# Optimization experiments

Hardware: AMD Instinct MI355X
Metric: run time of the kernel (lower is better)

## Reference

```python
import jax, jax.numpy as jnp
import numpy as np

TEMPERATURE = 100.0

def setup_inputs() -> dict:
    key = jax.random.key(0)
    n, d = 8192, 4096
    grad = jax.random.normal(key, (n, d), dtype=jnp.float32)
    return {"grad": grad}

def reference(grad) -> jnp.ndarray:
    # scores_i = sum_j (G @ G^T)_{ij} = G_i . (sum_j G_j)  -- avoids [n,n] gram
    colsum = jnp.sum(grad, axis=0)                 # [d]
    scores = grad @ colsum                         # [n]
    w = jax.nn.softmax(scores / TEMPERATURE, axis=0)  # softmax over rows (dim=0)
    # weighted row pooling: sum_i w_i * G_i -> [d]
    return w @ grad
```

## Files before the change

### kernel.cpp

```cpp
#include <hip/hip_runtime.h>
#include <math.h>

#define NROWS 8192
#define NCOLS 4096
#define TEMPERATURE 100.0f

#define ROW_CHUNKS 128
#define ROWS_PER_CHUNK (NROWS / ROW_CHUNKS)

__global__ __launch_bounds__(256)
void colsum_kernel(const float* __restrict__ g, float* __restrict__ colsum) {
    const int col  = (blockIdx.x * 256 + threadIdx.x) * 4;
    const int row0 = blockIdx.y * ROWS_PER_CHUNK;
    const float* p = g + (size_t)row0 * NCOLS + col;
    float4 acc = make_float4(0.f, 0.f, 0.f, 0.f);
    #pragma unroll 4
    for (int r = 0; r < ROWS_PER_CHUNK; ++r) {
        float4 v = *reinterpret_cast<const float4*>(p);
        acc.x += v.x; acc.y += v.y; acc.z += v.z; acc.w += v.w;
        p += NCOLS;
    }
    atomicAdd(&colsum[col + 0], acc.x);
    atomicAdd(&colsum[col + 1], acc.y);
    atomicAdd(&colsum[col + 2], acc.z);
    atomicAdd(&colsum[col + 3], acc.w);
}

__global__ __launch_bounds__(256)
void scores_kernel(const float* __restrict__ g, const float* __restrict__ colsum,
                   float* __restrict__ scores) {
    __shared__ float cs[NCOLS];
    for (int i = threadIdx.x; i < NCOLS / 4; i += 256) {
        reinterpret_cast<float4*>(cs)[i] =
            reinterpret_cast<const float4*>(colsum)[i];
    }
    __syncthreads();

    const int wave = threadIdx.x >> 6;
    const int lane = threadIdx.x & 63;
    const int row  = blockIdx.x * 4 + wave;
    const float* p = g + (size_t)row * NCOLS;

    float acc = 0.f;
    #pragma unroll
    for (int k = 0; k < NCOLS / 256; ++k) {
        const int c = k * 256 + lane * 4;
        float4 v = *reinterpret_cast<const float4*>(p + c);
        float4 w = *reinterpret_cast<const float4*>(cs + c);
        acc += v.x * w.x + v.y * w.y + v.z * w.z + v.w * w.w;
    }
    #pragma unroll
    for (int off = 32; off > 0; off >>= 1) acc += __shfl_xor(acc, off, 64);
    if (lane == 0) scores[row] = acc;
}

__global__ __launch_bounds__(1024)
void softmax_kernel(const float* __restrict__ scores, float* __restrict__ w) {
    __shared__ float red[16];
    const int tid = threadIdx.x;

    float local[8];
    float m = -INFINITY;
    #pragma unroll
    for (int k = 0; k < 8; ++k) {
        local[k] = scores[tid + k * 1024];
        m = fmaxf(m, local[k]);
    }
    #pragma unroll
    for (int off = 32; off > 0; off >>= 1) m = fmaxf(m, __shfl_xor(m, off, 64));
    if ((tid & 63) == 0) red[tid >> 6] = m;
    __syncthreads();
    float gm = red[0];
    #pragma unroll
    for (int i = 1; i < 16; ++i) gm = fmaxf(gm, red[i]);
    __syncthreads();

    float e[8];
    float s = 0.f;
    #pragma unroll
    for (int k = 0; k < 8; ++k) {
        e[k] = __expf((local[k] - gm) * (1.0f / TEMPERATURE));
        s += e[k];
    }
    #pragma unroll
    for (int off = 32; off > 0; off >>= 1) s += __shfl_xor(s, off, 64);
    if ((tid & 63) == 0) red[tid >> 6] = s;
    __syncthreads();
    float total = 0.f;
    #pragma unroll
    for (int i = 0; i < 16; ++i) total += red[i];

    const float inv = 1.0f / total;
    #pragma unroll
    for (int k = 0; k < 8; ++k) w[tid + k * 1024] = e[k] * inv;
}

__global__ __launch_bounds__(256)
void pool_kernel(const float* __restrict__ g, const float* __restrict__ w,
                 float* __restrict__ out) {
    const int col  = (blockIdx.x * 256 + threadIdx.x) * 4;
    const int row0 = blockIdx.y * ROWS_PER_CHUNK;
    const float* p = g + (size_t)row0 * NCOLS + col;
    float4 acc = make_float4(0.f, 0.f, 0.f, 0.f);
    #pragma unroll 4
    for (int r = 0; r < ROWS_PER_CHUNK; ++r) {
        const float wt = w[row0 + r];
        float4 v = *reinterpret_cast<const float4*>(p);
        acc.x += wt * v.x; acc.y += wt * v.y;
        acc.z += wt * v.z; acc.w += wt * v.w;
        p += NCOLS;
    }
    atomicAdd(&out[col + 0], acc.x);
    atomicAdd(&out[col + 1], acc.y);
    atomicAdd(&out[col + 2], acc.z);
    atomicAdd(&out[col + 3], acc.w);
}

extern "C" void kernel_launch(void* const* d_in, const int* in_sizes, int n_in,
                              void* d_out, int out_size, void* d_ws, size_t ws_size,
                              hipStream_t stream) {
    const float* grad = (const float*)d_in[0];
    float* out = (float*)d_out;

    float* colsum = (float*)d_ws;
    float* scores = colsum + NCOLS;
    float* wgt    = scores + NROWS;

    hipMemsetAsync(colsum, 0, NCOLS * sizeof(float), stream);
    hipMemsetAsync(out, 0, NCOLS * sizeof(float), stream);

    dim3 grid1(NCOLS / 1024, ROW_CHUNKS);
    colsum_kernel<<<grid1, 256, 0, stream>>>(grad, colsum);

    scores_kernel<<<NROWS / 4, 256, 0, stream>>>(grad, colsum, scores);

    softmax_kernel<<<1, 1024, 0, stream>>>(scores, wgt);

    pool_kernel<<<grid1, 256, 0, stream>>>(grad, wgt, out);
}
```

Measured before the change: 252.1 us.

## Replace atomic column reductions with partial-sum buffers plus separate reduce kernels

Column sums and the weighted pooling now use 2048 blocks of 16 rows each, and every block writes its own partial row into a workspace buffer. A dedicated reduce kernel then sums the 512 partials, which removes the float atomics and the two memsets. The scores kernel now processes two rows per wave, and the pool kernel stages its weights in shared memory. In exchange, each reduction adds an extra 8 MB partial-buffer write and read plus two more kernel launches.

Result: no change. 249.3 us (-1.1%).

```diff
diff --git a/kernel.cpp b/kernel.cpp
--- a/kernel.cpp
+++ b/kernel.cpp
@@ -3,55 +3,85 @@
 
 #define NROWS 8192
 #define NCOLS 4096
-#define TEMPERATURE 100.0f
+#define NCOLS4 (NCOLS / 4)
+#define TEMP_INV 0.01f
 
-#define ROW_CHUNKS 128
-#define ROWS_PER_CHUNK (NROWS / ROW_CHUNKS)
+#define STRIPS 4
+#define CHUNKS 512
+#define CHUNK_ROWS (NROWS / CHUNKS)
+#define STREAM_BLKS (STRIPS * CHUNKS)
 
 __global__ __launch_bounds__(256)
-void colsum_kernel(const float* __restrict__ g, float* __restrict__ colsum) {
-    const int col  = (blockIdx.x * 256 + threadIdx.x) * 4;
-    const int row0 = blockIdx.y * ROWS_PER_CHUNK;
-    const float* p = g + (size_t)row0 * NCOLS + col;
+void colsum_partial_kernel(const float* __restrict__ g,
+                           float* __restrict__ partial) {
+    const int strip = blockIdx.x & (STRIPS - 1);
+    const int chunk = blockIdx.x >> 2;
+    const int col   = strip * 1024 + threadIdx.x * 4;
+    const float* p  = g + (size_t)chunk * CHUNK_ROWS * NCOLS + col;
     float4 acc = make_float4(0.f, 0.f, 0.f, 0.f);
-    #pragma unroll 4
-    for (int r = 0; r < ROWS_PER_CHUNK; ++r) {
+    #pragma unroll
+    for (int r = 0; r < CHUNK_ROWS; ++r) {
         float4 v = *reinterpret_cast<const float4*>(p);
         acc.x += v.x; acc.y += v.y; acc.z += v.z; acc.w += v.w;
         p += NCOLS;
     }
-    atomicAdd(&colsum[col + 0], acc.x);
-    atomicAdd(&colsum[col + 1], acc.y);
-    atomicAdd(&colsum[col + 2], acc.z);
-    atomicAdd(&colsum[col + 3], acc.w);
+    *reinterpret_cast<float4*>(partial + (size_t)chunk * NCOLS + col) = acc;
+}
+
+__global__ __launch_bounds__(256)
+void reduce_kernel(const float* __restrict__ partial, float* __restrict__ dst) {
+    const int tid = threadIdx.x;
+    const int f4  = blockIdx.x * 16 + (tid & 15);
+    const int grp = tid >> 4;
+    const float4* p4 = reinterpret_cast<const float4*>(partial);
+    float4 acc = make_float4(0.f, 0.f, 0.f, 0.f);
+    for (int c = grp; c < CHUNKS; c += 16) {
+        float4 v = p4[(size_t)c * NCOLS4 + f4];
+        acc.x += v.x; acc.y += v.y; acc.z += v.z; acc.w += v.w;
+    }
+    __shared__ float4 red[256];
+    red[tid] = acc;
+    __syncthreads();
+    #pragma unroll
+    for (int s = 128; s >= 16; s >>= 1) {
+        if (tid < s) {
+            float4 o = red[tid + s];
+            red[tid].x += o.x; red[tid].y += o.y;
+            red[tid].z += o.z; red[tid].w += o.w;
+        }
+        __syncthreads();
+    }
+    if (tid < 16)
+        reinterpret_cast<float4*>(dst)[blockIdx.x * 16 + tid] = red[tid];
 }
 
 __global__ __launch_bounds__(256)
 void scores_kernel(const float* __restrict__ g, const float* __restrict__ colsum,
                    float* __restrict__ scores) {
-    __shared__ float cs[NCOLS];
-    for (int i = threadIdx.x; i < NCOLS / 4; i += 256) {
-        reinterpret_cast<float4*>(cs)[i] =
-            reinterpret_cast<const float4*>(colsum)[i];
-    }
+    __shared__ float4 cs4[NCOLS4];
+    for (int i = threadIdx.x; i < NCOLS4; i += 256)
+        cs4[i] = reinterpret_cast<const float4*>(colsum)[i];
     __syncthreads();
 
     const int wave = threadIdx.x >> 6;
     const int lane = threadIdx.x & 63;
-    const int row  = blockIdx.x * 4 + wave;
-    const float* p = g + (size_t)row * NCOLS;
-
-    float acc = 0.f;
     #pragma unroll
-    for (int k = 0; k < NCOLS / 256; ++k) {
-        const int c = k * 256 + lane * 4;
-        float4 v = *reinterpret_cast<const float4*>(p + c);
-        float4 w = *reinterpret_cast<const float4*>(cs + c);
-        acc += v.x * w.x + v.y * w.y + v.z * w.z + v.w * w.w;
+    for (int rr = 0; rr < 2; ++rr) {
+        const int row = blockIdx.x * 8 + wave * 2 + rr;
+        const float4* gp = reinterpret_cast<const float4*>(g)
+                         + (size_t)row * NCOLS4;
+        float acc = 0.f;
+        #pragma unroll
+        for (int k = 0; k < 16; ++k) {
+            const int idx = k * 64 + lane;
+            float4 v = gp[idx];
+            float4 c = cs4[idx];
+            acc += v.x * c.x + v.y * c.y + v.z * c.z + v.w * c.w;
+        }
+        #pragma unroll
+        for (int off = 32; off; off >>= 1) acc += __shfl_xor(acc, off, 64);
+        if (lane == 0) scores[row] = acc;
     }
-    #pragma unroll
-    for (int off = 32; off > 0; off >>= 1) acc += __shfl_xor(acc, off, 64);
-    if (lane == 0) scores[row] = acc;
 }
 
 __global__ __launch_bounds__(1024)
@@ -67,7 +97,7 @@
         m = fmaxf(m, local[k]);
     }
     #pragma unroll
-    for (int off = 32; off > 0; off >>= 1) m = fmaxf(m, __shfl_xor(m, off, 64));
+    for (int off = 32; off; off >>= 1) m = fmaxf(m, __shfl_xor(m, off, 64));
     if ((tid & 63) == 0) red[tid >> 6] = m;
     __syncthreads();
     float gm = red[0];
@@ -79,11 +109,11 @@
     float s = 0.f;
     #pragma unroll
     for (int k = 0; k < 8; ++k) {
-        e[k] = __expf((local[k] - gm) * (1.0f / TEMPERATURE));
+        e[k] = __expf((local[k] - gm) * TEMP_INV);
         s += e[k];
     }
     #pragma unroll
-    for (int off = 32; off > 0; off >>= 1) s += __shfl_xor(s, off, 64);
+    for (int off = 32; off; off >>= 1) s += __shfl_xor(s, off, 64);
     if ((tid & 63) == 0) red[tid >> 6] = s;
     __syncthreads();
     float total = 0.f;
@@ -96,24 +126,28 @@
 }
 
 __global__ __launch_bounds__(256)
-void pool_kernel(const float* __restrict__ g, const float* __restrict__ w,
-                 float* __restrict__ out) {
-    const int col  = (blockIdx.x * 256 + threadIdx.x) * 4;
-    const int row0 = blockIdx.y * ROWS_PER_CHUNK;
-    const float* p = g + (size_t)row0 * NCOLS + col;
+void pool_partial_kernel(const float* __restrict__ g, const float* __restrict__ w,
+                         float* __restrict__ partial) {
+    const int strip = blockIdx.x & (STRIPS - 1);
+    const int chunk = blockIdx.x >> 2;
+
+    __shared__ float wsm[CHUNK_ROWS];
+    if (threadIdx.x < CHUNK_ROWS)
+        wsm[threadIdx.x] = w[chunk * CHUNK_ROWS + threadIdx.x];
+    __syncthreads();
+
+    const int col  = strip * 1024 + threadIdx.x * 4;
+    const float* p = g + (size_t)chunk * CHUNK_ROWS * NCOLS + col;
     float4 acc = make_float4(0.f, 0.f, 0.f, 0.f);
-    #pragma unroll 4
-    for (int r = 0; r < ROWS_PER_CHUNK; ++r) {
-        const float wt = w[row0 + r];
+    #pragma unroll
+    for (int r = 0; r < CHUNK_ROWS; ++r) {
+        const float wt = wsm[r];
         float4 v = *reinterpret_cast<const float4*>(p);
         acc.x += wt * v.x; acc.y += wt * v.y;
         acc.z += wt * v.z; acc.w += wt * v.w;
         p += NCOLS;
     }
-    atomicAdd(&out[col + 0], acc.x);
-    atomicAdd(&out[col + 1], acc.y);
-    atomicAdd(&out[col + 2], acc.z);
-    atomicAdd(&out[col + 3], acc.w);
+    *reinterpret_cast<float4*>(partial + (size_t)chunk * NCOLS + col) = acc;
 }
 
 extern "C" void kernel_launch(void* const* d_in, const int* in_sizes, int n_in,
@@ -122,19 +156,15 @@
     const float* grad = (const float*)d_in[0];
     float* out = (float*)d_out;
 
-    float* colsum = (float*)d_ws;
-    float* scores = colsum + NCOLS;
-    float* wgt    = scores + NROWS;
+    float* partial = (float*)d_ws;
+    float* colsum  = partial + (size_t)CHUNKS * NCOLS;
+    float* scores  = colsum + NCOLS;
+    float* wgt     = scores + NROWS;
 
-    hipMemsetAsync(colsum, 0, NCOLS * sizeof(float), stream);
-    hipMemsetAsync(out, 0, NCOLS * sizeof(float), stream);
-
-    dim3 grid1(NCOLS / 1024, ROW_CHUNKS);
-    colsum_kernel<<<grid1, 256, 0, stream>>>(grad, colsum);
-
-    scores_kernel<<<NROWS / 4, 256, 0, stream>>>(grad, colsum, scores);
-
+    colsum_partial_kernel<<<STREAM_BLKS, 256, 0, stream>>>(grad, partial);
+    reduce_kernel<<<64, 256, 0, stream>>>(partial, colsum);
+    scores_kernel<<<NROWS / 8, 256, 0, stream>>>(grad, colsum, scores);
     softmax_kernel<<<1, 1024, 0, stream>>>(scores, wgt);
-
-    pool_kernel<<<grid1, 256, 0, stream>>>(grad, wgt, out);
+    pool_partial_kernel<<<STREAM_BLKS, 256, 0, stream>>>(grad, wgt, partial);
+    reduce_kernel<<<64, 256, 0, stream>>>(partial, out);
 }
```
